# Optimization experiments

Measured on AMD Instinct MI355X. Metric: run time of the kernel, lower is better.

## Reference

```python
import jax, jax.numpy as jnp
import numpy as np

N = 100000      # num nodes
E = 3200000     # num edges (avg degree 32)
F = 512         # num_features
D = 256         # args.dim
C = 64          # num_classes
K = 10          # APPNP iterations
ALPHA = 0.1


def setup_inputs() -> dict:
    key = jax.random.key(0)
    ks = jax.random.split(key, 6)
    x = jax.random.normal(ks[0], (N, F), dtype=jnp.float32)
    edge_index = jax.random.randint(ks[1], (2, E), 0, N, dtype=jnp.int64)
    edge_weight_train = jax.random.normal(ks[2], (E,), dtype=jnp.float32)
    x_weight = jnp.ones((F,), dtype=jnp.float32)
    W1 = jax.random.normal(ks[3], (F, D), dtype=jnp.float32) * 0.02
    b1 = jnp.zeros((D,), dtype=jnp.float32)
    W2 = jax.random.normal(ks[4], (D, C), dtype=jnp.float32) * 0.02
    b2 = jnp.zeros((C,), dtype=jnp.float32)
    return {"x": x, "edge_index": edge_index, "edge_weight_train": edge_weight_train,
            "x_weight": x_weight, "W1": W1, "b1": b1, "W2": W2, "b2": b2}


def reference(x, edge_index, edge_weight_train, x_weight, W1, b1, W2, b2):
    row, col = edge_index[0], edge_index[1]
    # adj_sparse branch: mask edges with |w|==0, weight = sigmoid(w).
    # Filtering edges == zeroing their weight (degrees and messages scale by w).
    edge_mask = jnp.abs(edge_weight_train) > 0
    w = jnp.where(edge_mask, jax.nn.sigmoid(edge_weight_train), 0.0)
    # gcn_norm with self-loops (fill value 1.0)
    loop = jnp.arange(N, dtype=row.dtype)
    row2 = jnp.concatenate([row, loop])
    col2 = jnp.concatenate([col, loop])
    w2 = jnp.concatenate([w, jnp.ones((N,), dtype=w.dtype)])
    deg = jax.ops.segment_sum(w2, col2, num_segments=N)
    dinv = jnp.where(deg > 0, jax.lax.rsqrt(jnp.maximum(deg, 1e-12)), 0.0)
    norm = dinv[row2] * w2 * dinv[col2]  # [E+N]

    # feature_sparse branch
    x_mask = (jnp.abs(x_weight) > 0).astype(x.dtype)
    xw = jax.nn.sigmoid(x_weight) * x_mask
    xin = x * xw  # broadcast over nodes

    h = jax.nn.relu(xin @ W1 + b1)          # [N, D] (dropout is eval no-op)
    z0 = h @ W2 + b2                        # [N, C]

    z = z0
    for _ in range(K):
        msg = z[row2] * norm[:, None]       # gather + scale, [E+N, C]
        agg = jax.ops.segment_sum(msg, col2, num_segments=N)
        z = (1.0 - ALPHA) * agg + ALPHA * z0
    return jax.nn.log_softmax(z, axis=1)
```

## Files before the change

kernel.cpp:

```cpp
#include <hip/hip_runtime.h>
#include <hip/hip_bf16.h>
#include <cstdint>
#include <cstddef>

#define ALPHA 0.1f
#define K_ITERS 10
#define NPART 8

typedef __attribute__((ext_vector_type(8))) short bf16x8;
typedef __attribute__((ext_vector_type(4))) float f32x4;
typedef __attribute__((ext_vector_type(4))) unsigned int u32x4;

#define U15INV (1.0f / 32767.0f)

__device__ __forceinline__ unsigned short f2bf(float f) {
    unsigned int u = __float_as_uint(f);
    u += 0x7fffu + ((u >> 16) & 1u);
    return (unsigned short)(u >> 16);
}
__device__ __forceinline__ float bflo(unsigned int u) {
    return __uint_as_float(u << 16);
}
__device__ __forceinline__ float bfhi(unsigned int u) {
    return __uint_as_float(u & 0xffff0000u);
}
__device__ __forceinline__ unsigned int pack2(float a, float b) {
    return (unsigned int)f2bf(a) | ((unsigned int)f2bf(b) << 16);
}
__device__ __forceinline__ unsigned int u15q(float w) {
    return (unsigned int)(w * 32767.0f + 0.5f);
}
__device__ __forceinline__ int xcd_id() {
    unsigned int x;
    asm volatile("s_getreg_b32 %0, hwreg(20, 0, 32)" : "=s"(x));
    return (int)(x & (NPART - 1));
}


__global__ __launch_bounds__(256) void setup_k(int* cntp, unsigned int* cs, int* flag,
                                               int ncnt, int ncs) {
    int i = blockIdx.x * 256 + threadIdx.x;
    if (i == 0) *flag = 0;
    if (i < ncnt) cntp[i] = 0;
    if (i < ncs) cs[i] = 0;
}

__global__ void detect_idx_k(const void* ei, int* flag, int E_, int N_) {
    int tid = threadIdx.x;
    const long long* p = (const long long*)ei;
    int bad = 0;
    int lim = (E_ < 4096) ? E_ : 4096;
    for (int i = tid; i < lim; i += 256) {
        long long v = p[i];
        if (v < 0 || v >= (long long)N_) bad = 1;
    }
    if (bad) atomicOr(flag, 1);
}

__global__ __launch_bounds__(256) void prep_edges_k(const void* ei, const float* ew,
                                                    unsigned long long* epack, int* cntp,
                                                    const int* flag, int E_, int N_) {
    int e = blockIdx.x * 256 + threadIdx.x;
    if (e >= E_) return;
    int is32 = *flag;
    unsigned long long r, c;
    if (is32) {
        const int* p = (const int*)ei;
        r = (unsigned long long)(unsigned int)__builtin_nontemporal_load(&p[e]);
        c = (unsigned long long)(unsigned int)__builtin_nontemporal_load(&p[(size_t)E_ + e]);
    } else {
        const long long* p = (const long long*)ei;
        r = (unsigned long long)__builtin_nontemporal_load(&p[e]);
        c = (unsigned long long)__builtin_nontemporal_load(&p[(size_t)E_ + e]);
    }
    float t = __builtin_nontemporal_load(&ew[e]);
    float wv = (fabsf(t) > 0.0f) ? 1.0f / (1.0f + expf(-t)) : 0.0f;
    unsigned long long part = (unsigned long long)xcd_id();
    unsigned long long rk = (unsigned long long)(unsigned int)
        __hip_atomic_fetch_add(&cntp[(size_t)part * N_ + (int)c], 1,
                               __ATOMIC_RELAXED, __HIP_MEMORY_SCOPE_WORKGROUP);
    unsigned long long v = r | (c << 17) | ((unsigned long long)u15q(wv) << 34)
                             | (part << 49) | (rk << 52);
    __builtin_nontemporal_store(v, &epack[e]);
}

__global__ __launch_bounds__(256) void combine_k(const int* cntp, int* pofs, int* cnt8, int N_) {
    int i = blockIdx.x * 256 + threadIdx.x;
    if (i >= N_) return;
    int s = 0;
    #pragma unroll
    for (int p = 0; p < NPART; ++p) {
        size_t idx = (size_t)p * N_ + i;
        int v = cntp[idx];
        pofs[idx] = s;
        s += v;
    }
    cnt8[i] = (s + 7) & ~7;
}

__global__ __launch_bounds__(256) void scan1_k(const int* cnt, int* bsum, int N_) {
    __shared__ int sm[256];
    int t = threadIdx.x, i = blockIdx.x * 256 + t;
    sm[t] = (i < N_) ? cnt[i] : 0;
    __syncthreads();
    for (int off = 128; off; off >>= 1) {
        if (t < off) sm[t] += sm[t + off];
        __syncthreads();
    }
    if (t == 0) bsum[blockIdx.x] = sm[0];
}

__global__ __launch_bounds__(1024) void scan2_k(const int* bsum, int* boff, int nb) {
    __shared__ int sm[1024];
    int t = threadIdx.x;
    int v = (t < nb) ? bsum[t] : 0;
    sm[t] = v;
    __syncthreads();
    for (int off = 1; off < 1024; off <<= 1) {
        int x = (t >= off) ? sm[t - off] : 0;
        __syncthreads();
        sm[t] += x;
        __syncthreads();
    }
    if (t < nb) boff[t] = sm[t] - v;
}

__global__ __launch_bounds__(256) void scan3_k(const int* cnt, const int* boff, int* rowstart, int N_) {
    __shared__ int sm[256];
    int t = threadIdx.x, i = blockIdx.x * 256 + t;
    int v = (i < N_) ? cnt[i] : 0;
    sm[t] = v;
    __syncthreads();
    for (int off = 1; off < 256; off <<= 1) {
        int x = (t >= off) ? sm[t - off] : 0;
        __syncthreads();
        sm[t] += x;
        __syncthreads();
    }
    if (i < N_)  rowstart[i]  = boff[blockIdx.x] + sm[t] - v;
    if (i == N_ - 1) rowstart[N_] = boff[blockIdx.x] + sm[t];
}

__global__ __launch_bounds__(256) void fill_csr_k(const unsigned long long* epack, const int* pofs,
                                                  const int* rowstart, unsigned int* cs,
                                                  int E_, int N_) {
    int e = blockIdx.x * 256 + threadIdx.x;
    if (e >= E_) return;
    unsigned long long v = __builtin_nontemporal_load(&epack[e]);
    unsigned int r   = (unsigned int)(v & 0x1ffffu);
    int          c   = (int)((v >> 17) & 0x1ffffu);
    unsigned int w15 = (unsigned int)((v >> 34) & 0x7fffu);
    int         part = (int)((v >> 49) & 7u);
    int           rk = (int)(v >> 52);
    int pos = rowstart[c] + pofs[(size_t)part * N_ + c] + rk;
    cs[pos] = r | (w15 << 17);
}

__global__ __launch_bounds__(256) void deg_dinv_k(const unsigned int* __restrict__ cs,
                                                  const int* __restrict__ rowstart,
                                                  float* __restrict__ dinv, int N_) {
    int node = blockIdx.x * 8 + (threadIdx.x >> 5);
    int l = threadIdx.x & 31;
    if (node >= N_) return;
    int s = rowstart[node], e = rowstart[node + 1];
    float sum = 0.0f;
    for (int j = s + l; j < e; j += 32) sum += (float)(cs[j] >> 17) * U15INV;
    #pragma unroll
    for (int off = 16; off; off >>= 1) sum += __shfl_xor(sum, off, 64);
    float d = sum + 1.0f;
    if (l == 0) dinv[node] = (d > 0.0f) ? rsqrtf(fmaxf(d, 1e-12f)) : 0.0f;
}

__global__ __launch_bounds__(256) void norm_k(unsigned int* __restrict__ cs,
                                              const int* __restrict__ rowstart,
                                              const float* __restrict__ dinv, int N_) {
    int node = blockIdx.x * 8 + (threadIdx.x >> 5);
    int l = threadIdx.x & 31;
    if (node >= N_) return;
    int s = rowstart[node], e = rowstart[node + 1];
    float dc = dinv[node];
    for (int j = s + l; j < e; j += 32) {
        unsigned int v = cs[j];
        unsigned int src = v & 0x1ffffu;
        float w = (float)(v >> 17) * U15INV;
        float nm = dinv[src] * w * dc;
        cs[j] = src | (u15q(nm) << 17);
    }
}

__global__ __launch_bounds__(256) void wprep_k(const float* W1, const float* xw, unsigned short* W1bT,
                                               const float* W2, unsigned short* W2bT,
                                               int F_, int D_, int C_) {
    int i = blockIdx.x * 256 + threadIdx.x;
    int n1 = F_ * D_;
    if (i < n1) {
        int k = i / D_, n = i % D_;
        float t = xw[k];
        float s = (fabsf(t) > 0.0f) ? 1.0f / (1.0f + expf(-t)) : 0.0f;
        W1bT[(size_t)n * F_ + k] = f2bf(W1[i] * s);
    } else if (i < n1 + D_ * C_) {
        int j = i - n1;
        int k = j / C_, n = j % C_;
        W2bT[(size_t)n * D_ + k] = f2bf(W2[j]);
    }
}

__global__ __launch_bounds__(512) void gemm1_512_k(const float* __restrict__ A,
                                                   const unsigned short* __restrict__ BT,
                                                   const float* __restrict__ bias,
                                                   unsigned short* __restrict__ C,
                                                   int M, int K, int Nn) {
    const int BK = 32;
    __shared__ __align__(16) unsigned short Asl[2][4][128][8];
    __shared__ __align__(16) unsigned short Bsl[2][4][256][8];

    int tid = threadIdx.x;
    int row0 = blockIdx.x * 128;
    int wid = tid >> 6, lane = tid & 63;
    int wm = wid & 1, wn = wid >> 1;
    int lrow = lane & 15, kg = lane >> 4;

    f32x4 acc[4][4];
    #pragma unroll
    for (int i = 0; i < 4; ++i)
        #pragma unroll
        for (int j = 0; j < 4; ++j) acc[i][j] = (f32x4){0.f, 0.f, 0.f, 0.f};

    int ar = tid >> 2, akg = tid & 3;
    int agrow = row0 + ar;
    bool avalid = agrow < M;
    int bn_ = tid >> 1, bkh = (tid & 1) * 16;

    float fa[8];
    bf16x8 bv0, bv1;

    auto loadTile = [&](int k0) {
        if (avalid) {
            const f32x4* p = (const f32x4*)&A[(size_t)agrow * K + k0 + akg * 8];
            *(f32x4*)&fa[0] = p[0];
            *(f32x4*)&fa[4] = p[1];
        }
        const bf16x8* p = (const bf16x8*)&BT[(size_t)bn_ * K + k0 + bkh];
        bv0 = p[0]; bv1 = p[1];
    };
    auto stageTile = [&](int buf) {
        unsigned short av[8];
        #pragma unroll
        for (int q = 0; q < 8; ++q) av[q] = avalid ? f2bf(fa[q]) : (unsigned short)0;
        *(bf16x8*)&Asl[buf][akg][ar][0] = *(bf16x8*)&av[0];
        *(bf16x8*)&Bsl[buf][(bkh >> 3) + 0][bn_][0] = bv0;
        *(bf16x8*)&Bsl[buf][(bkh >> 3) + 1][bn_][0] = bv1;
    };

    int nsteps = K / BK;
    loadTile(0);
    stageTile(0);
    __syncthreads();

    int cur = 0;
    for (int step = 0; step < nsteps; ++step) {
        bool more = (step + 1) < nsteps;
        if (more) loadTile((step + 1) * BK);

        bf16x8 af[4], bfr[4];
        #pragma unroll
        for (int i = 0; i < 4; ++i)
            af[i] = *(bf16x8*)&Asl[cur][kg][wm * 64 + i * 16 + lrow][0];
        #pragma unroll
        for (int j = 0; j < 4; ++j)
            bfr[j] = *(bf16x8*)&Bsl[cur][kg][wn * 64 + j * 16 + lrow][0];
        #pragma unroll
        for (int i = 0; i < 4; ++i)
            #pragma unroll
            for (int j = 0; j < 4; ++j)
                acc[i][j] = __builtin_amdgcn_mfma_f32_16x16x32_bf16(af[i], bfr[j], acc[i][j], 0, 0, 0);

        if (more) stageTile(cur ^ 1);
        __syncthreads();
        cur ^= 1;
    }

    #pragma unroll
    for (int i = 0; i < 4; ++i) {
        #pragma unroll
        for (int j = 0; j < 4; ++j) {
            int col = wn * 64 + j * 16 + lrow;
            float bv = bias[col];
            #pragma unroll
            for (int r = 0; r < 4; ++r) {
                int grow = row0 + wm * 64 + i * 16 + kg * 4 + r;
                if (grow < M) {
                    float v = fmaxf(acc[i][j][r] + bv, 0.0f);
                    C[(size_t)grow * Nn + col] = f2bf(v);
                }
            }
        }
    }
}

__global__ __launch_bounds__(256) void gemm2_k(const unsigned short* __restrict__ Ab,
                                               const unsigned short* __restrict__ BT,
                                               const float* __restrict__ bias,
                                               unsigned short* __restrict__ C,
                                               int M, int K, int Nn) {
    const int BN = 64, BK = 32;
    __shared__ __align__(16) unsigned short Asl[2][4][128][8];
    __shared__ __align__(16) unsigned short Bsl[2][4][BN][8];

    int tid = threadIdx.x;
    int row0 = blockIdx.x * 128;
    int wid = tid >> 6, lane = tid & 63;
    int wm = wid & 1, wn = wid >> 1;
    const int NT = BN / 32;
    int lrow = lane & 15, kg = lane >> 4;

    f32x4 acc[4][NT];
    #pragma unroll
    for (int i = 0; i < 4; ++i)
        #pragma unroll
        for (int j = 0; j < NT; ++j) acc[i][j] = (f32x4){0.f, 0.f, 0.f, 0.f};

    int ar = tid >> 1, akh = (tid & 1) * 16;
    int agrow = row0 + ar;
    bool avalid = agrow < M;
    int bn_ = tid >> 1, bkh = (tid & 1) * 16;
    bool bvalid = bn_ < BN;

    unsigned short ha[16];
    bf16x8 bv0, bv1;

    auto loadTile = [&](int k0) {
        if (avalid) {
            const bf16x8* p = (const bf16x8*)&Ab[(size_t)agrow * K + k0 + akh];
            *(bf16x8*)&ha[0] = p[0];
            *(bf16x8*)&ha[8] = p[1];
        }
        if (bvalid) {
            const bf16x8* p = (const bf16x8*)&BT[(size_t)bn_ * K + k0 + bkh];
            bv0 = p[0]; bv1 = p[1];
        }
    };
    auto stageTile = [&](int buf) {
        unsigned short av[16];
        #pragma unroll
        for (int q = 0; q < 16; ++q) av[q] = avalid ? ha[q] : (unsigned short)0;
        *(bf16x8*)&Asl[buf][(akh >> 3) + 0][ar][0] = *(bf16x8*)&av[0];
        *(bf16x8*)&Asl[buf][(akh >> 3) + 1][ar][0] = *(bf16x8*)&av[8];
        if (bvalid) {
            *(bf16x8*)&Bsl[buf][(bkh >> 3) + 0][bn_][0] = bv0;
            *(bf16x8*)&Bsl[buf][(bkh >> 3) + 1][bn_][0] = bv1;
        }
    };

    int nsteps = K / BK;
    loadTile(0);
    stageTile(0);
    __syncthreads();

    int cur = 0;
    for (int step = 0; step < nsteps; ++step) {
        bool more = (step + 1) < nsteps;
        if (more) loadTile((step + 1) * BK);

        bf16x8 af[4], bfr[NT];
        #pragma unroll
        for (int i = 0; i < 4; ++i)
            af[i] = *(bf16x8*)&Asl[cur][kg][wm * 64 + i * 16 + lrow][0];
        #pragma unroll
        for (int j = 0; j < NT; ++j)
            bfr[j] = *(bf16x8*)&Bsl[cur][kg][wn * (BN / 2) + j * 16 + lrow][0];
        #pragma unroll
        for (int i = 0; i < 4; ++i)
            #pragma unroll
            for (int j = 0; j < NT; ++j)
                acc[i][j] = __builtin_amdgcn_mfma_f32_16x16x32_bf16(af[i], bfr[j], acc[i][j], 0, 0, 0);

        if (more) stageTile(cur ^ 1);
        __syncthreads();
        cur ^= 1;
    }

    #pragma unroll
    for (int i = 0; i < 4; ++i) {
        #pragma unroll
        for (int j = 0; j < NT; ++j) {
            int col = wn * (BN / 2) + j * 16 + lrow;
            float bv = bias[col];
            #pragma unroll
            for (int r = 0; r < 4; ++r) {
                int grow = row0 + wm * 64 + i * 16 + kg * 4 + r;
                if (grow < M)
                    C[(size_t)grow * Nn + col] = f2bf(acc[i][j][r] + bv);
            }
        }
    }
}

template<bool LAST>
__global__ __launch_bounds__(256) void prop8_k(const unsigned short* __restrict__ z,
                                               const unsigned short* __restrict__ z0,
                                               const int* __restrict__ rowstart,
                                               const unsigned int* __restrict__ cs,
                                               const float* __restrict__ dinv,
                                               unsigned short* __restrict__ znew,
                                               float* __restrict__ out, int N_) {
    int node = blockIdx.x * 32 + (threadIdx.x >> 3);
    int l = threadIdx.x & 7;
    if (node >= N_) return;
    int s = rowstart[node], e = rowstart[node + 1];
    float d = dinv[node];
    size_t ro = (size_t)node * 64 + l * 8;
    u32x4 zs = *(const u32x4*)&z[ro];
    float dd = d * d;
    float a[8];
    a[0] = dd * bflo(zs.x); a[1] = dd * bfhi(zs.x);
    a[2] = dd * bflo(zs.y); a[3] = dd * bfhi(zs.y);
    a[4] = dd * bflo(zs.z); a[5] = dd * bfhi(zs.z);
    a[6] = dd * bflo(zs.w); a[7] = dd * bfhi(zs.w);

    for (int j = s; j < e; j += 8) {
        u32x4 p0 = __builtin_nontemporal_load((const u32x4*)&cs[j]);
        u32x4 p1 = __builtin_nontemporal_load((const u32x4*)&cs[j + 4]);
        unsigned int pe[8] = { p0.x, p0.y, p0.z, p0.w, p1.x, p1.y, p1.z, p1.w };
        u32x4 g[8];
        #pragma unroll
        for (int q = 0; q < 8; ++q)
            g[q] = *(const u32x4*)&z[(size_t)(pe[q] & 0x1ffffu) * 64 + l * 8];
        #pragma unroll
        for (int q = 0; q < 8; ++q) {
            float w = (float)(pe[q] >> 17) * U15INV;
            a[0] += w * bflo(g[q].x); a[1] += w * bfhi(g[q].x);
            a[2] += w * bflo(g[q].y); a[3] += w * bfhi(g[q].y);
            a[4] += w * bflo(g[q].z); a[5] += w * bfhi(g[q].z);
            a[6] += w * bflo(g[q].w); a[7] += w * bfhi(g[q].w);
        }
    }

    u32x4 z0v = __builtin_nontemporal_load((const u32x4*)&z0[ro]);
    float v[8];
    float z0f[8] = { bflo(z0v.x), bfhi(z0v.x), bflo(z0v.y), bfhi(z0v.y),
                     bflo(z0v.z), bfhi(z0v.z), bflo(z0v.w), bfhi(z0v.w) };
    #pragma unroll
    for (int q = 0; q < 8; ++q) v[q] = (1.0f - ALPHA) * a[q] + ALPHA * z0f[q];

    if (!LAST) {
        u32x4 o;
        o.x = pack2(v[0], v[1]); o.y = pack2(v[2], v[3]);
        o.z = pack2(v[4], v[5]); o.w = pack2(v[6], v[7]);
        *(u32x4*)&znew[ro] = o;
    } else {
        float m = v[0];
        #pragma unroll
        for (int q = 1; q < 8; ++q) m = fmaxf(m, v[q]);
        #pragma unroll
        for (int off = 1; off < 8; off <<= 1) m = fmaxf(m, __shfl_xor(m, off, 64));
        float sum = 0.0f;
        #pragma unroll
        for (int q = 0; q < 8; ++q) sum += expf(v[q] - m);
        #pragma unroll
        for (int off = 1; off < 8; off <<= 1) sum += __shfl_xor(sum, off, 64);
        float lg = logf(sum);
        float4 o0 = make_float4(v[0] - m - lg, v[1] - m - lg, v[2] - m - lg, v[3] - m - lg);
        float4 o1 = make_float4(v[4] - m - lg, v[5] - m - lg, v[6] - m - lg, v[7] - m - lg);
        *(float4*)&out[ro] = o0;
        *(float4*)&out[ro + 4] = o1;
    }
}


extern "C" void kernel_launch(void* const* d_in, const int* in_sizes, int n_in,
                              void* d_out, int out_size, void* d_ws, size_t ws_size,
                              hipStream_t stream) {
    const float* x   = (const float*)d_in[0];
    const void*  ei  = d_in[1];
    const float* ew  = (const float*)d_in[2];
    const float* xw  = (const float*)d_in[3];
    const float* W1  = (const float*)d_in[4];
    const float* b1  = (const float*)d_in[5];
    const float* W2  = (const float*)d_in[6];
    const float* b2  = (const float*)d_in[7];

    const int F_ = in_sizes[3];
    const int N_ = in_sizes[0] / F_;
    const int E_ = in_sizes[2];
    const int D_ = in_sizes[5];
    const int C_ = in_sizes[7];

    const int E8 = E_ + 7 * N_;

    char* base = (char*)d_ws;
    size_t off = 0;
    auto take = [&](size_t bytes) -> void* {
        void* p = base + off;
        off += (bytes + 255) & ~(size_t)255;
        return p;
    };
    unsigned long long* epack = (unsigned long long*)take((size_t)E_ * 8);
    unsigned int* cs = (unsigned int*)take((size_t)E8 * 4);
    int*   cntp     = (int*)  take((size_t)NPART * N_ * 4);
    int*   pofs     = (int*)  take((size_t)NPART * N_ * 4);
    int*   cnt8     = (int*)  take((size_t)N_ * 4);
    float* dinv     = (float*)take((size_t)N_ * 4);
    int*   rowstart = (int*)  take((size_t)(N_ + 1) * 4);
    int*   flag     = (int*)  take(256);
    int*   bsum     = (int*)  take(4096 * 4);
    int*   boff     = (int*)  take(4096 * 4);
    unsigned short* W1bT = (unsigned short*)take((size_t)F_ * D_ * 2);
    unsigned short* W2bT = (unsigned short*)take((size_t)D_ * C_ * 2);
    unsigned short* h    = (unsigned short*)take((size_t)N_ * D_ * 2);
    unsigned short* z0b  = (unsigned short*)take((size_t)N_ * C_ * 2);
    unsigned short* za   = (unsigned short*)take((size_t)N_ * C_ * 2);
    unsigned short* zb   = (unsigned short*)take((size_t)N_ * C_ * 2);

    (void)ws_size; (void)n_in; (void)out_size;

    int nblk = (N_ + 255) / 256;
    int eblk = (E_ + 255) / 256;
    int ncnt = NPART * N_;
    int setup_blk = ((ncnt > E8 ? ncnt : E8) + 255) / 256;

    setup_k<<<setup_blk, 256, 0, stream>>>(cntp, cs, flag, ncnt, E8);
    detect_idx_k<<<1, 256, 0, stream>>>(ei, flag, E_, N_);
    prep_edges_k<<<eblk, 256, 0, stream>>>(ei, ew, epack, cntp, flag, E_, N_);
    combine_k<<<nblk, 256, 0, stream>>>(cntp, pofs, cnt8, N_);
    scan1_k<<<nblk, 256, 0, stream>>>(cnt8, bsum, N_);
    scan2_k<<<1, 1024, 0, stream>>>(bsum, boff, nblk);
    scan3_k<<<nblk, 256, 0, stream>>>(cnt8, boff, rowstart, N_);
    fill_csr_k<<<eblk, 256, 0, stream>>>(epack, pofs, rowstart, cs, E_, N_);
    int gblk8 = (N_ + 7) / 8;
    deg_dinv_k<<<gblk8, 256, 0, stream>>>(cs, rowstart, dinv, N_);
    norm_k<<<gblk8, 256, 0, stream>>>(cs, rowstart, dinv, N_);
    wprep_k<<<(F_ * D_ + D_ * C_ + 255) / 256, 256, 0, stream>>>(W1, xw, W1bT, W2, W2bT, F_, D_, C_);

    int gx = (N_ + 127) / 128;
    gemm1_512_k<<<gx, 512, 0, stream>>>(x, W1bT, b1, h, N_, F_, D_);
    gemm2_k<<<gx, 256, 0, stream>>>(h, W2bT, b2, z0b, N_, D_, C_);

    int pblk = (N_ + 31) / 32;
    const unsigned short* cur = z0b;
    unsigned short* bufs[2] = { za, zb };
    for (int it = 0; it < K_ITERS - 1; ++it) {
        unsigned short* dst = bufs[it & 1];
        prop8_k<false><<<pblk, 256, 0, stream>>>(cur, z0b, rowstart, cs, dinv, dst, nullptr, N_);
        cur = dst;
    }
    prop8_k<true><<<pblk, 256, 0, stream>>>(cur, z0b, rowstart, cs, dinv, nullptr, (float*)d_out, N_);
}
```

Measured before the change: 932.8 us.

## Fuse second GEMM into first GEMM epilogue via shared memory

The hidden activation tile from the first GEMM (bias plus ReLU, in bf16) is now written into reused shared memory, and the second GEMM against W2 is computed in the same kernel. This removes the global write and read of the N×D hidden buffer and one kernel launch. The price is a longer kernel with an extra barrier and W2 operands read straight from global memory. Separately, nontemporal load and store hints are dropped from the edge preparation and CSR fill kernels.

```diff
diff --git a/kernel.cpp b/kernel.cpp
--- a/kernel.cpp
+++ b/kernel.cpp
@@ -66,22 +66,21 @@
     unsigned long long r, c;
     if (is32) {
         const int* p = (const int*)ei;
-        r = (unsigned long long)(unsigned int)__builtin_nontemporal_load(&p[e]);
-        c = (unsigned long long)(unsigned int)__builtin_nontemporal_load(&p[(size_t)E_ + e]);
+        r = (unsigned long long)(unsigned int)p[e];
+        c = (unsigned long long)(unsigned int)p[(size_t)E_ + e];
     } else {
         const long long* p = (const long long*)ei;
-        r = (unsigned long long)__builtin_nontemporal_load(&p[e]);
-        c = (unsigned long long)__builtin_nontemporal_load(&p[(size_t)E_ + e]);
-    }
-    float t = __builtin_nontemporal_load(&ew[e]);
+        r = (unsigned long long)p[e];
+        c = (unsigned long long)p[(size_t)E_ + e];
+    }
+    float t = ew[e];
     float wv = (fabsf(t) > 0.0f) ? 1.0f / (1.0f + expf(-t)) : 0.0f;
     unsigned long long part = (unsigned long long)xcd_id();
     unsigned long long rk = (unsigned long long)(unsigned int)
         __hip_atomic_fetch_add(&cntp[(size_t)part * N_ + (int)c], 1,
                                __ATOMIC_RELAXED, __HIP_MEMORY_SCOPE_WORKGROUP);
-    unsigned long long v = r | (c << 17) | ((unsigned long long)u15q(wv) << 34)
-                             | (part << 49) | (rk << 52);
-    __builtin_nontemporal_store(v, &epack[e]);
+    epack[e] = r | (c << 17) | ((unsigned long long)u15q(wv) << 34)
+                 | (part << 49) | (rk << 52);
 }
 
 __global__ __launch_bounds__(256) void combine_k(const int* cntp, int* pofs, int* cnt8, int N_) {
@@ -146,7 +145,7 @@
                                                   int E_, int N_) {
     int e = blockIdx.x * 256 + threadIdx.x;
     if (e >= E_) return;
-    unsigned long long v = __builtin_nontemporal_load(&epack[e]);
+    unsigned long long v = epack[e];
     unsigned int r   = (unsigned int)(v & 0x1ffffu);
     int          c   = (int)((v >> 17) & 0x1ffffu);
     unsigned int w15 = (unsigned int)((v >> 34) & 0x7fffu);
@@ -205,14 +204,19 @@
     }
 }
 
-__global__ __launch_bounds__(512) void gemm1_512_k(const float* __restrict__ A,
-                                                   const unsigned short* __restrict__ BT,
-                                                   const float* __restrict__ bias,
-                                                   unsigned short* __restrict__ C,
-                                                   int M, int K, int Nn) {
+__global__ __launch_bounds__(512) void gemm_fused_k(const float* __restrict__ A,
+                                                    const unsigned short* __restrict__ BT,
+                                                    const float* __restrict__ b1,
+                                                    const unsigned short* __restrict__ W2bT,
+                                                    const float* __restrict__ b2,
+                                                    unsigned short* __restrict__ z0out,
+                                                    int M, int K, int Nn, int Cn) {
     const int BK = 32;
-    __shared__ __align__(16) unsigned short Asl[2][4][128][8];
-    __shared__ __align__(16) unsigned short Bsl[2][4][256][8];
+    __shared__ __align__(16) unsigned short SMEM[32768];
+    typedef unsigned short (*AslT)[4][128][8];
+    typedef unsigned short (*BslT)[4][256][8];
+    AslT Asl = (AslT)SMEM;
+    BslT Bsl = (BslT)(SMEM + 8192);
 
     int tid = threadIdx.x;
     int row0 = blockIdx.x * 128;
@@ -284,114 +288,42 @@
     for (int i = 0; i < 4; ++i) {
         #pragma unroll
         for (int j = 0; j < 4; ++j) {
-            int col = wn * 64 + j * 16 + lrow;
-            float bv = bias[col];
+            int k2 = wn * 64 + j * 16 + lrow;
+            float bv = b1[k2];
+            int base = ((k2 >> 5) * 4 + ((k2 >> 3) & 3)) * 1024 + (k2 & 7);
             #pragma unroll
             for (int r = 0; r < 4; ++r) {
-                int grow = row0 + wm * 64 + i * 16 + kg * 4 + r;
-                if (grow < M) {
-                    float v = fmaxf(acc[i][j][r] + bv, 0.0f);
-                    C[(size_t)grow * Nn + col] = f2bf(v);
-                }
+                int row = wm * 64 + i * 16 + kg * 4 + r;
+                float v = fmaxf(acc[i][j][r] + bv, 0.0f);
+                SMEM[base + row * 8] = f2bf(v);
             }
         }
     }
-}
-
-__global__ __launch_bounds__(256) void gemm2_k(const unsigned short* __restrict__ Ab,
-                                               const unsigned short* __restrict__ BT,
-                                               const float* __restrict__ bias,
-                                               unsigned short* __restrict__ C,
-                                               int M, int K, int Nn) {
-    const int BN = 64, BK = 32;
-    __shared__ __align__(16) unsigned short Asl[2][4][128][8];
-    __shared__ __align__(16) unsigned short Bsl[2][4][BN][8];
-
-    int tid = threadIdx.x;
-    int row0 = blockIdx.x * 128;
-    int wid = tid >> 6, lane = tid & 63;
-    int wm = wid & 1, wn = wid >> 1;
-    const int NT = BN / 32;
-    int lrow = lane & 15, kg = lane >> 4;
-
-    f32x4 acc[4][NT];
-    #pragma unroll
-    for (int i = 0; i < 4; ++i)
-        #pragma unroll
-        for (int j = 0; j < NT; ++j) acc[i][j] = (f32x4){0.f, 0.f, 0.f, 0.f};
-
-    int ar = tid >> 1, akh = (tid & 1) * 16;
-    int agrow = row0 + ar;
-    bool avalid = agrow < M;
-    int bn_ = tid >> 1, bkh = (tid & 1) * 16;
-    bool bvalid = bn_ < BN;
-
-    unsigned short ha[16];
-    bf16x8 bv0, bv1;
-
-    auto loadTile = [&](int k0) {
-        if (avalid) {
-            const bf16x8* p = (const bf16x8*)&Ab[(size_t)agrow * K + k0 + akh];
-            *(bf16x8*)&ha[0] = p[0];
-            *(bf16x8*)&ha[8] = p[1];
-        }
-        if (bvalid) {
-            const bf16x8* p = (const bf16x8*)&BT[(size_t)bn_ * K + k0 + bkh];
-            bv0 = p[0]; bv1 = p[1];
-        }
-    };
-    auto stageTile = [&](int buf) {
-        unsigned short av[16];
-        #pragma unroll
-        for (int q = 0; q < 16; ++q) av[q] = avalid ? ha[q] : (unsigned short)0;
-        *(bf16x8*)&Asl[buf][(akh >> 3) + 0][ar][0] = *(bf16x8*)&av[0];
-        *(bf16x8*)&Asl[buf][(akh >> 3) + 1][ar][0] = *(bf16x8*)&av[8];
-        if (bvalid) {
-            *(bf16x8*)&Bsl[buf][(bkh >> 3) + 0][bn_][0] = bv0;
-            *(bf16x8*)&Bsl[buf][(bkh >> 3) + 1][bn_][0] = bv1;
-        }
-    };
-
-    int nsteps = K / BK;
-    loadTile(0);
-    stageTile(0);
     __syncthreads();
 
-    int cur = 0;
-    for (int step = 0; step < nsteps; ++step) {
-        bool more = (step + 1) < nsteps;
-        if (more) loadTile((step + 1) * BK);
-
-        bf16x8 af[4], bfr[NT];
+    f32x4 acc2[4];
+    #pragma unroll
+    for (int i = 0; i < 4; ++i) acc2[i] = (f32x4){0.f, 0.f, 0.f, 0.f};
+    int col2 = wn * 16 + lrow;
+    #pragma unroll
+    for (int ch = 0; ch < 8; ++ch) {
+        bf16x8 bfr2 = *(const bf16x8*)&W2bT[(size_t)col2 * Nn + ch * 32 + kg * 8];
+        bf16x8 af2[4];
         #pragma unroll
         for (int i = 0; i < 4; ++i)
-            af[i] = *(bf16x8*)&Asl[cur][kg][wm * 64 + i * 16 + lrow][0];
-        #pragma unroll
-        for (int j = 0; j < NT; ++j)
-            bfr[j] = *(bf16x8*)&Bsl[cur][kg][wn * (BN / 2) + j * 16 + lrow][0];
+            af2[i] = *(bf16x8*)&SMEM[(ch * 4 + kg) * 1024 + (wm * 64 + i * 16 + lrow) * 8];
         #pragma unroll
         for (int i = 0; i < 4; ++i)
-            #pragma unroll
-            for (int j = 0; j < NT; ++j)
-                acc[i][j] = __builtin_amdgcn_mfma_f32_16x16x32_bf16(af[i], bfr[j], acc[i][j], 0, 0, 0);
-
-        if (more) stageTile(cur ^ 1);
-        __syncthreads();
-        cur ^= 1;
-    }
-
+            acc2[i] = __builtin_amdgcn_mfma_f32_16x16x32_bf16(af2[i], bfr2, acc2[i], 0, 0, 0);
+    }
+    float bv2 = b2[col2];
     #pragma unroll
     for (int i = 0; i < 4; ++i) {
         #pragma unroll
-        for (int j = 0; j < NT; ++j) {
-            int col = wn * (BN / 2) + j * 16 + lrow;
-            float bv = bias[col];
-            #pragma unroll
-            for (int r = 0; r < 4; ++r) {
-                int grow = row0 + wm * 64 + i * 16 + kg * 4 + r;
-                if (grow < M)
-                    C[(size_t)grow * Nn + col] = f2bf(acc[i][j][r] + bv);
-            }
+        for (int r = 0; r < 4; ++r) {
+            int grow = row0 + wm * 64 + i * 16 + kg * 4 + r;
+            if (grow < M)
+                z0out[(size_t)grow * Cn + col2] = f2bf(acc2[i][r] + bv2);
         }
     }
 }
@@ -507,7 +439,6 @@
     int*   boff     = (int*)  take(4096 * 4);
     unsigned short* W1bT = (unsigned short*)take((size_t)F_ * D_ * 2);
     unsigned short* W2bT = (unsigned short*)take((size_t)D_ * C_ * 2);
-    unsigned short* h    = (unsigned short*)take((size_t)N_ * D_ * 2);
     unsigned short* z0b  = (unsigned short*)take((size_t)N_ * C_ * 2);
     unsigned short* za   = (unsigned short*)take((size_t)N_ * C_ * 2);
     unsigned short* zb   = (unsigned short*)take((size_t)N_ * C_ * 2);
@@ -533,8 +464,7 @@
     wprep_k<<<(F_ * D_ + D_ * C_ + 255) / 256, 256, 0, stream>>>(W1, xw, W1bT, W2, W2bT, F_, D_, C_);
 
     int gx = (N_ + 127) / 128;
-    gemm1_512_k<<<gx, 512, 0, stream>>>(x, W1bT, b1, h, N_, F_, D_);
-    gemm2_k<<<gx, 256, 0, stream>>>(h, W2bT, b2, z0b, N_, D_, C_);
+    gemm_fused_k<<<gx, 512, 0, stream>>>(x, W1bT, b1, W2bT, b2, z0b, N_, F_, D_, C_);
 
     int pblk = (N_ + 31) / 32;
     const unsigned short* cur = z0b;
```

Measured after the change: 875.0 us. 6.2% less time.
